# Kernel optimization log

Hardware: AMD Instinct MI355X
Metric: run time of the kernel (lower is better)

Reference implementation:

```python
import jax, jax.numpy as jnp
import numpy as np

WORD_LEN = 4094
MAX_LEN = 9
EMB = 512
HID = 256
BATCH = 32768


def setup_inputs() -> dict:
    key = jax.random.key(0)
    ks = jax.random.split(key, 16)
    s = 0.02
    return {
        "decode_word": jax.random.randint(ks[0], (BATCH, 1), 0, WORD_LEN),
        "hidden": jax.random.normal(ks[1], (BATCH, HID), jnp.float32),
        "encoder_output": jax.random.normal(ks[2], (BATCH, MAX_LEN, HID), jnp.float32),
        "emb_table": jax.random.normal(ks[3], (WORD_LEN, EMB), jnp.float32) * s,
        "atten_W": jax.random.normal(ks[4], (MAX_LEN, 2 * HID), jnp.float32) * s,
        "atten_b": jnp.zeros((MAX_LEN,), jnp.float32),
        "comb_W": jax.random.normal(ks[5], (EMB, EMB + HID), jnp.float32) * s,
        "comb_b": jnp.zeros((EMB,), jnp.float32),
        "W_ih": jax.random.normal(ks[6], (3 * HID, EMB), jnp.float32) * s,
        "b_ih": jnp.zeros((3 * HID,), jnp.float32),
        "W_hh": jax.random.normal(ks[7], (3 * HID, HID), jnp.float32) * s,
        "b_hh": jnp.zeros((3 * HID,), jnp.float32),
        "out_W": jax.random.normal(ks[8], (WORD_LEN, HID), jnp.float32) * s,
        "out_b": jnp.zeros((WORD_LEN,), jnp.float32),
    }


def reference(decode_word, hidden, encoder_output, emb_table, atten_W, atten_b,
              comb_W, comb_b, W_ih, b_ih, W_hh, b_hh, out_W, out_b):
    # embedding: [B,1,E]
    embedded = emb_table[decode_word]
    B = hidden.shape[0]
    # expand hidden to [B,L,H], concat with encoder_output -> attention scores [B,L,L]
    hx = jnp.broadcast_to(hidden[:, None, :], (B, MAX_LEN, HID))
    scores = jnp.einsum('blf,mf->blm', jnp.concatenate([encoder_output, hx], axis=2), atten_W) + atten_b
    atten_weight = jax.nn.softmax(scores, axis=2)
    # bmm: [B,L,L] @ [B,L,H] -> [B,L,H], then sum over L -> context [B,1,H]
    atten_applied = jnp.einsum('blm,bmh->blh', atten_weight, encoder_output)
    c_i = atten_applied.sum(axis=1)[:, None, :]
    # combine + relu: [B,1,E]
    x = jnp.concatenate([embedded, c_i], axis=2) @ comb_W.T + comb_b
    x = jax.nn.relu(x)[:, 0]  # [B,E]
    # GRUCell (PyTorch gate order: r, z, n)
    gi = x @ W_ih.T + b_ih
    gh = hidden @ W_hh.T + b_hh
    i_r, i_z, i_n = jnp.split(gi, 3, axis=1)
    h_r, h_z, h_n = jnp.split(gh, 3, axis=1)
    r = jax.nn.sigmoid(i_r + h_r)
    z = jax.nn.sigmoid(i_z + h_z)
    n = jnp.tanh(i_n + r * h_n)
    h_new = (1.0 - z) * n + z * hidden
    # output projection + log_softmax over vocab
    out = jax.nn.log_softmax(h_new @ out_W.T + out_b, axis=1)
    return out, h_new
```

## Files before the change

### kernel.cpp

```cpp
#include <hip/hip_runtime.h>

typedef __bf16 bf16x8 __attribute__((ext_vector_type(8)));
typedef float  f32x4  __attribute__((ext_vector_type(4)));

#define BATCH_ 32768
#define VOC 4094
#define LGT_STRIDE 8188

__device__ inline unsigned short f2bf(float f) {
    unsigned int u = __builtin_bit_cast(unsigned int, f);
    unsigned int r = u + 0x7FFFu + ((u >> 16) & 1u);
    return (unsigned short)(r >> 16);
}
__device__ inline float bf2f(unsigned short u) {
    unsigned int v = ((unsigned int)u) << 16;
    return __builtin_bit_cast(float, v);
}
__device__ inline f32x4 mfma16(bf16x8 a, bf16x8 b, f32x4 c) {
    return __builtin_amdgcn_mfma_f32_16x16x32_bf16(a, b, c, 0, 0, 0);
}
__device__ inline void gload16(const void* g, void* l) {
    __builtin_amdgcn_global_load_lds(
        (const __attribute__((address_space(1))) void*)(g),
        (__attribute__((address_space(3))) void*)(l),
        16, 0, 0);
}

__global__ __launch_bounds__(256) void k_prep(
    const float* __restrict__ comb_W, const float* __restrict__ W_ih,
    const float* __restrict__ W_hh, const float* __restrict__ out_W,
    const float* __restrict__ b_ih, const float* __restrict__ b_hh,
    const float* __restrict__ out_b,
    unsigned short* __restrict__ cwb, unsigned short* __restrict__ wg2,
    unsigned short* __restrict__ owb, float* __restrict__ bg,
    float* __restrict__ obp) {
    int i = blockIdx.x * 256 + threadIdx.x;
    if (i < 512 * 768) {
        int n = i / 768, k = i - n * 768;
        int by = n >> 7, r = n & 127, kc = k >> 7, kl = k & 127;
        int dst = (by * 6 + kc) * 16384 + r * 128 + (((kl >> 3) ^ (r & 7)) << 3) + (kl & 7);
        cwb[dst] = f2bf(comb_W[i]);
    }
    if (i < 1024 * 768) {
        int row = i / 768, k = i - row * 768;
        int hgrp = row >> 6, g = (row >> 4) & 3, hl = row & 15;
        int h = hgrp * 16 + hl;
        float v;
        if (g == 0) v = (k < 512) ? W_ih[(size_t)h * 512 + k] : W_hh[(size_t)h * 256 + (k - 512)];
        else if (g == 1) v = (k < 512) ? W_ih[(size_t)(256 + h) * 512 + k] : W_hh[(size_t)(256 + h) * 256 + (k - 512)];
        else if (g == 2) v = (k < 512) ? W_ih[(size_t)(512 + h) * 512 + k] : 0.f;
        else v = (k < 512) ? 0.f : W_hh[(size_t)(512 + h) * 256 + (k - 512)];
        int by = row >> 7, r = row & 127, kc = k >> 7, kl = k & 127;
        int dst = (by * 6 + kc) * 16384 + r * 128 + (((kl >> 3) ^ (r & 7)) << 3) + (kl & 7);
        wg2[dst] = f2bf(v);
    }
    if (i < 4096 * 256) {
        int n = i >> 8, k = i & 255;
        int by = n >> 7, r = n & 127, kc = k >> 7, kl = k & 127;
        int dst = (by * 2 + kc) * 16384 + r * 128 + (((kl >> 3) ^ (r & 7)) << 3) + (kl & 7);
        owb[dst] = (n < VOC) ? f2bf(out_W[i]) : (unsigned short)0;
    }
    if (i < 1024) {
        float v = (i < 512) ? (b_ih[i] + b_hh[i]) : ((i < 768) ? b_ih[i] : b_hh[i - 256]);
        bg[i] = v;
    }
    if (i < 4096) obp[i] = (i < VOC) ? out_b[i] : -1.0e30f;
}

__global__ __launch_bounds__(256) void k_attn(
    const int* __restrict__ dw, const float* __restrict__ hidden,
    const float* __restrict__ enc, const float* __restrict__ emb,
    const float* __restrict__ aW, const float* __restrict__ ab,
    unsigned short* __restrict__ xcat, unsigned short* __restrict__ xh) {
    __shared__ float sAW[9 * 516];
    __shared__ float sAB[9];
    int tid = threadIdx.x;
    for (int i = tid; i < 9 * 512; i += 256) {
        int m = i >> 9, k = i & 511;
        sAW[m * 516 + k] = aW[i];
    }
    if (tid < 9) sAB[tid] = ab[tid];
    __syncthreads();
    int w = tid >> 6, lane = tid & 63;
    int b = blockIdx.x * 4 + w;
    const float* encb = enc + (size_t)b * (9 * 256);
    float4 h4 = *(const float4*)(hidden + (size_t)b * 256 + 4 * lane);

    float4 e[9];
#pragma unroll
    for (int l = 0; l < 9; l++) e[l] = *(const float4*)(encb + l * 256 + 4 * lane);

    float u[9];
#pragma unroll
    for (int m = 0; m < 9; m++) {
        float4 a = *(const float4*)&sAW[m * 516 + 256 + 4 * lane];
        float v = h4.x * a.x + h4.y * a.y + h4.z * a.z + h4.w * a.w;
        v += __shfl_xor(v, 1);  v += __shfl_xor(v, 2);  v += __shfl_xor(v, 4);
        v += __shfl_xor(v, 8);  v += __shfl_xor(v, 16); v += __shfl_xor(v, 32);
        u[m] = v + sAB[m];
    }
    float wsum[9] = {0, 0, 0, 0, 0, 0, 0, 0, 0};
#pragma unroll
    for (int l = 0; l < 9; l++) {
        float p[9];
#pragma unroll
        for (int m = 0; m < 9; m++) {
            float4 a = *(const float4*)&sAW[m * 516 + 4 * lane];
            float v = e[l].x * a.x + e[l].y * a.y + e[l].z * a.z + e[l].w * a.w;
            v += __shfl_xor(v, 1);  v += __shfl_xor(v, 2);  v += __shfl_xor(v, 4);
            v += __shfl_xor(v, 8);  v += __shfl_xor(v, 16); v += __shfl_xor(v, 32);
            p[m] = v + u[m];
        }
        float mx = p[0];
#pragma unroll
        for (int m = 1; m < 9; m++) mx = fmaxf(mx, p[m]);
        float s = 0.f, ex[9];
#pragma unroll
        for (int m = 0; m < 9; m++) { ex[m] = __expf(p[m] - mx); s += ex[m]; }
        float inv = 1.f / s;
#pragma unroll
        for (int m = 0; m < 9; m++) wsum[m] += ex[m] * inv;
    }
    float c0 = 0, c1 = 0, c2 = 0, c3 = 0;
#pragma unroll
    for (int m = 0; m < 9; m++) {
        c0 += wsum[m] * e[m].x; c1 += wsum[m] * e[m].y;
        c2 += wsum[m] * e[m].z; c3 += wsum[m] * e[m].w;
    }
    ushort4 cb; cb.x = f2bf(c0); cb.y = f2bf(c1); cb.z = f2bf(c2); cb.w = f2bf(c3);
    *(ushort4*)(xcat + (size_t)b * 768 + 512 + 4 * lane) = cb;
    ushort4 hb; hb.x = f2bf(h4.x); hb.y = f2bf(h4.y); hb.z = f2bf(h4.z); hb.w = f2bf(h4.w);
    *(ushort4*)(xh + (size_t)b * 768 + 512 + 4 * lane) = hb;

    int word = dw[b];
    const float* er = emb + (size_t)word * 512 + 8 * lane;
    float4 e0 = *(const float4*)er;
    float4 e1 = *(const float4*)(er + 4);
    ushort4 w0; w0.x = f2bf(e0.x); w0.y = f2bf(e0.y); w0.z = f2bf(e0.z); w0.w = f2bf(e0.w);
    ushort4 w1; w1.x = f2bf(e1.x); w1.y = f2bf(e1.y); w1.z = f2bf(e1.z); w1.w = f2bf(e1.w);
    *(ushort4*)(xcat + (size_t)b * 768 + 8 * lane) = w0;
    *(ushort4*)(xcat + (size_t)b * 768 + 8 * lane + 4) = w1;
}

__global__ __launch_bounds__(256, 2) void k_combine(
    const unsigned short* __restrict__ xcat, const unsigned short* __restrict__ cwb,
    const float* __restrict__ comb_b, unsigned short* __restrict__ xh) {
    __shared__ __align__(16) char smem[65536];
    int wgid = blockIdx.x;
    int xcd = wgid & 7, slot = wgid >> 3;
    int bx = xcd * 32 + (slot & 31), by = slot >> 5;
    int tid = threadIdx.x, w = tid >> 6, lane = tid & 63;
    int lo = lane & 15, hi = lane >> 4;
    int bm0 = bx * 128, n0 = by * 128;
    const __bf16* A = (const __bf16*)xcat;
    const char* gb = (const char*)cwb + (size_t)by * 6 * 32768;
    f32x4 acc[2][8] = {};
    bf16x8 Afb[2][2][4];
#pragma unroll
    for (int mf = 0; mf < 2; mf++)
#pragma unroll
        for (int ks = 0; ks < 4; ks++)
            Afb[0][mf][ks] = *(const bf16x8*)(A + (size_t)(bm0 + w * 32 + mf * 16 + lo) * 768 + ks * 32 + 8 * hi);
    for (int it = 0; it < 8; it++) {
        int uo = ((w * 8 + it) << 10);
        gload16(gb + uo + lane * 16, smem + uo);
    }
    __syncthreads();
#pragma unroll
    for (int c = 0; c < 6; c++) {
        if (c < 5) {
#pragma unroll
            for (int mf = 0; mf < 2; mf++)
#pragma unroll
                for (int ks = 0; ks < 4; ks++)
                    Afb[(c + 1) & 1][mf][ks] = *(const bf16x8*)(A + (size_t)(bm0 + w * 32 + mf * 16 + lo) * 768 + (c + 1) * 128 + ks * 32 + 8 * hi);
            const char* gc = gb + (size_t)(c + 1) * 32768;
            int boff = ((c + 1) & 1) * 32768;
            for (int it = 0; it < 8; it++) {
                int uo = ((w * 8 + it) << 10);
                gload16(gc + uo + lane * 16, smem + boff + uo);
            }
            __builtin_amdgcn_sched_barrier(0);
        }
        int cb0 = (c & 1) * 32768;
#pragma unroll
        for (int ks = 0; ks < 4; ks++)
#pragma unroll
            for (int nf = 0; nf < 8; nf++) {
                int row = nf * 16 + lo;
                bf16x8 bfr = *(const bf16x8*)(smem + cb0 + row * 256 + (((ks * 4 + hi) ^ (lo & 7)) << 4));
                acc[0][nf] = mfma16(Afb[c & 1][0][ks], bfr, acc[0][nf]);
                acc[1][nf] = mfma16(Afb[c & 1][1][ks], bfr, acc[1][nf]);
            }
        __syncthreads();
    }
#pragma unroll
    for (int mf = 0; mf < 2; mf++)
#pragma unroll
        for (int nf = 0; nf < 8; nf++) {
            int col = n0 + nf * 16 + lo;
            float cb = comb_b[col];
#pragma unroll
            for (int r = 0; r < 4; r++) {
                int row = bm0 + w * 32 + mf * 16 + hi * 4 + r;
                xh[(size_t)row * 768 + col] = f2bf(fmaxf(acc[mf][nf][r] + cb, 0.f));
            }
        }
}

__global__ __launch_bounds__(256, 2) void k_gru(
    const unsigned short* __restrict__ xh, const unsigned short* __restrict__ wg2,
    const float* __restrict__ bg, const float* __restrict__ hidden,
    float* __restrict__ hnew_out, unsigned short* __restrict__ hnb) {
    __shared__ __align__(16) char smem[65536];
    int wgid = blockIdx.x;
    int xcd = wgid & 7, slot = wgid >> 3;
    int bx = xcd * 32 + (slot & 31), by = slot >> 5;
    int tid = threadIdx.x, w = tid >> 6, lane = tid & 63;
    int lo = lane & 15, hi = lane >> 4;
    int bm0 = bx * 128;
    int h00 = by * 32;
    const __bf16* A = (const __bf16*)xh;
    const char* gb = (const char*)wg2 + (size_t)by * 6 * 32768;
    f32x4 acc[2][8] = {};
    bf16x8 Afb[2][2][4];
#pragma unroll
    for (int mf = 0; mf < 2; mf++)
#pragma unroll
        for (int ks = 0; ks < 4; ks++)
            Afb[0][mf][ks] = *(const bf16x8*)(A + (size_t)(bm0 + w * 32 + mf * 16 + lo) * 768 + ks * 32 + 8 * hi);
    for (int it = 0; it < 8; it++) {
        int uo = ((w * 8 + it) << 10);
        gload16(gb + uo + lane * 16, smem + uo);
    }
    __syncthreads();
#pragma unroll
    for (int c = 0; c < 6; c++) {
        if (c < 5) {
#pragma unroll
            for (int mf = 0; mf < 2; mf++)
#pragma unroll
                for (int ks = 0; ks < 4; ks++)
                    Afb[(c + 1) & 1][mf][ks] = *(const bf16x8*)(A + (size_t)(bm0 + w * 32 + mf * 16 + lo) * 768 + (c + 1) * 128 + ks * 32 + 8 * hi);
            const char* gc = gb + (size_t)(c + 1) * 32768;
            int boff = ((c + 1) & 1) * 32768;
            for (int it = 0; it < 8; it++) {
                int uo = ((w * 8 + it) << 10);
                gload16(gc + uo + lane * 16, smem + boff + uo);
            }
            __builtin_amdgcn_sched_barrier(0);
        }
        int cb0 = (c & 1) * 32768;
#pragma unroll
        for (int ks = 0; ks < 4; ks++)
#pragma unroll
            for (int nf = 0; nf < 8; nf++) {
                int row = nf * 16 + lo;
                bf16x8 bfr = *(const bf16x8*)(smem + cb0 + row * 256 + (((ks * 4 + hi) ^ (lo & 7)) << 4));
                acc[0][nf] = mfma16(Afb[c & 1][0][ks], bfr, acc[0][nf]);
                acc[1][nf] = mfma16(Afb[c & 1][1][ks], bfr, acc[1][nf]);
            }
        __syncthreads();
    }
#pragma unroll
    for (int mf = 0; mf < 2; mf++)
#pragma unroll
        for (int hgrp = 0; hgrp < 2; hgrp++) {
            int col = h00 + hgrp * 16 + lo;
            float br = bg[col], bz = bg[256 + col], bi = bg[512 + col], bh = bg[768 + col];
#pragma unroll
            for (int r = 0; r < 4; r++) {
                int row = bm0 + w * 32 + mf * 16 + hi * 4 + r;
                float rr = 1.f / (1.f + __expf(-(acc[mf][hgrp * 4 + 0][r] + br)));
                float zz = 1.f / (1.f + __expf(-(acc[mf][hgrp * 4 + 1][r] + bz)));
                float nn = tanhf(acc[mf][hgrp * 4 + 2][r] + bi + rr * (acc[mf][hgrp * 4 + 3][r] + bh));
                float hp = hidden[(size_t)row * 256 + col];
                float hn = zz * (hp - nn) + nn;
                hnew_out[(size_t)row * 256 + col] = hn;
                hnb[(size_t)row * 256 + col] = f2bf(hn);
            }
        }
}

__global__ __launch_bounds__(256, 2) void k_logit(
    const unsigned short* __restrict__ hnb, const unsigned short* __restrict__ owb,
    const float* __restrict__ obp, unsigned short* __restrict__ lgt,
    float* __restrict__ psum) {
    __shared__ __align__(16) char smem[65536];
    int wgid = blockIdx.x;
    int xcd = wgid & 7, slot = wgid >> 3;
    int bx = xcd * 32 + (slot & 31), by = slot >> 5;
    int tid = threadIdx.x, w = tid >> 6, lane = tid & 63;
    int lo = lane & 15, hi = lane >> 4;
    int bm0 = bx * 128, n0 = by * 128;
    const __bf16* A = (const __bf16*)hnb;
    const char* gb = (const char*)owb + (size_t)by * 2 * 32768;

    for (int it = 0; it < 8; it++) {
        int uo = ((w * 8 + it) << 10);
        gload16(gb + uo + lane * 16, smem + uo);
    }
    bf16x8 Af[2][8];
#pragma unroll
    for (int mf = 0; mf < 2; mf++)
#pragma unroll
        for (int ks = 0; ks < 8; ks++)
            Af[mf][ks] = *(const bf16x8*)(A + (size_t)(bm0 + w * 32 + mf * 16 + lo) * 256 + ks * 32 + 8 * hi);
    __syncthreads();
    for (int it = 0; it < 8; it++) {
        int uo = ((w * 8 + it) << 10);
        gload16(gb + 32768 + uo + lane * 16, smem + 32768 + uo);
    }
    __builtin_amdgcn_sched_barrier(0);

    f32x4 acc[2][8] = {};
#pragma unroll
    for (int ks = 0; ks < 4; ks++)
#pragma unroll
        for (int nf = 0; nf < 8; nf++) {
            int row = nf * 16 + lo;
            bf16x8 bfr = *(const bf16x8*)(smem + row * 256 + (((ks * 4 + hi) ^ (lo & 7)) << 4));
            acc[0][nf] = mfma16(Af[0][ks], bfr, acc[0][nf]);
            acc[1][nf] = mfma16(Af[1][ks], bfr, acc[1][nf]);
        }
    __syncthreads();
#pragma unroll
    for (int ks = 4; ks < 8; ks++)
#pragma unroll
        for (int nf = 0; nf < 8; nf++) {
            int row = nf * 16 + lo;
            bf16x8 bfr = *(const bf16x8*)(smem + 32768 + row * 256 + ((((ks - 4) * 4 + hi) ^ (lo & 7)) << 4));
            acc[0][nf] = mfma16(Af[0][ks], bfr, acc[0][nf]);
            acc[1][nf] = mfma16(Af[1][ks], bfr, acc[1][nf]);
        }
    __syncthreads();

    unsigned short* T = (unsigned short*)smem;
    float se[2][4] = {};
#pragma unroll
    for (int mf = 0; mf < 2; mf++)
#pragma unroll
        for (int nf = 0; nf < 8; nf++) {
            int col = n0 + nf * 16 + lo;
            float ob = obp[col];
#pragma unroll
            for (int r = 0; r < 4; r++) {
                float lg = acc[mf][nf][r] + ob;
                se[mf][r] += __expf(lg);
                T[(w * 32 + mf * 16 + hi * 4 + r) * 136 + nf * 16 + lo] = f2bf(lg);
            }
        }
#pragma unroll
    for (int mf = 0; mf < 2; mf++)
#pragma unroll
        for (int r = 0; r < 4; r++) {
            float v = se[mf][r];
            v += __shfl_xor(v, 1); v += __shfl_xor(v, 2);
            v += __shfl_xor(v, 4); v += __shfl_xor(v, 8);
            se[mf][r] = v;
        }
    if (lo == 0) {
#pragma unroll
        for (int mf = 0; mf < 2; mf++)
#pragma unroll
            for (int r = 0; r < 4; r++)
                psum[(size_t)by * BATCH_ + bm0 + w * 32 + mf * 16 + hi * 4 + r] = se[mf][r];
    }
    __syncthreads();
#pragma unroll
    for (int it = 0; it < 8; it++) {
        int t = it * 256 + tid;
        int row = t >> 4, ch = t & 15;
        ushort4 a = *(ushort4*)(T + row * 136 + ch * 8);
        ushort4 b = *(ushort4*)(T + row * 136 + ch * 8 + 4);
        size_t base = (size_t)(bm0 + row) * LGT_STRIDE + n0 + ch * 8;
        *(ushort4*)(lgt + base) = a;
        *(ushort4*)(lgt + base + 4) = b;
    }
}

__global__ __launch_bounds__(256) void k_lse(
    const float* __restrict__ psum, float* __restrict__ lse) {
    int b = blockIdx.x * 256 + threadIdx.x;
    float t = 0.f;
#pragma unroll
    for (int s = 0; s < 32; s++) t += psum[(size_t)s * BATCH_ + b];
    lse[b] = __logf(t);
}

__global__ __launch_bounds__(256) void k_out2(
    const float* __restrict__ lse, float* __restrict__ out) {
    int b = blockIdx.x, tid = threadIdx.x;
    float l = lse[b];
    const unsigned short* rowp = (const unsigned short*)(out + (size_t)b * VOC);
    ushort4 a0 = *(const ushort4*)(rowp + tid * 8);
    ushort4 b0 = *(const ushort4*)(rowp + tid * 8 + 4);
    ushort4 a1 = *(const ushort4*)(rowp + 2048 + tid * 8);
    ushort4 b1 = *(const ushort4*)(rowp + 2048 + tid * 8 + 4);
    __syncthreads();
    float* orow = out + (size_t)b * VOC;
    int v0 = tid * 8;
    {
        float2 p;
        p.x = bf2f(a0.x) - l; p.y = bf2f(a0.y) - l; *(float2*)(orow + v0) = p;
        p.x = bf2f(a0.z) - l; p.y = bf2f(a0.w) - l; *(float2*)(orow + v0 + 2) = p;
        p.x = bf2f(b0.x) - l; p.y = bf2f(b0.y) - l; *(float2*)(orow + v0 + 4) = p;
        p.x = bf2f(b0.z) - l; p.y = bf2f(b0.w) - l; *(float2*)(orow + v0 + 6) = p;
    }
    int v1 = 2048 + tid * 8;
    {
        float2 p;
        p.x = bf2f(a1.x) - l; p.y = bf2f(a1.y) - l;
        if (v1 + 1 < VOC) *(float2*)(orow + v1) = p;
        p.x = bf2f(a1.z) - l; p.y = bf2f(a1.w) - l;
        if (v1 + 3 < VOC) *(float2*)(orow + v1 + 2) = p;
        p.x = bf2f(b1.x) - l; p.y = bf2f(b1.y) - l;
        if (v1 + 5 < VOC) *(float2*)(orow + v1 + 4) = p;
        p.x = bf2f(b1.z) - l; p.y = bf2f(b1.w) - l;
        if (v1 + 7 < VOC) *(float2*)(orow + v1 + 6) = p;
    }
}

extern "C" void kernel_launch(void* const* d_in, const int* in_sizes, int n_in,
                              void* d_out, int out_size, void* d_ws, size_t ws_size,
                              hipStream_t stream) {
    const int*   dw      = (const int*)d_in[0];
    const float* hidden  = (const float*)d_in[1];
    const float* enc     = (const float*)d_in[2];
    const float* emb     = (const float*)d_in[3];
    const float* aW      = (const float*)d_in[4];
    const float* ab      = (const float*)d_in[5];
    const float* comb_W  = (const float*)d_in[6];
    const float* comb_b  = (const float*)d_in[7];
    const float* W_ih    = (const float*)d_in[8];
    const float* b_ih    = (const float*)d_in[9];
    const float* W_hh    = (const float*)d_in[10];
    const float* b_hh    = (const float*)d_in[11];
    const float* out_W   = (const float*)d_in[12];
    const float* out_b   = (const float*)d_in[13];

    float* out = (float*)d_out;
    float* hnew_out = out + (size_t)BATCH_ * VOC;

    unsigned short* xcat = (unsigned short*)d_ws;
    unsigned short* xh   = xcat + (size_t)BATCH_ * 768;
    unsigned short* hnb  = xh + (size_t)BATCH_ * 768;
    float* psum          = (float*)(hnb + (size_t)BATCH_ * 256);
    float* lse           = psum + (size_t)32 * BATCH_;
    float* obp           = lse + BATCH_;
    unsigned short* cwb  = (unsigned short*)(obp + 4096);
    unsigned short* wg2  = cwb + 512 * 768;
    unsigned short* owb  = wg2 + 1024 * 768;
    float* bg            = (float*)(owb + 4096 * 256);

    k_prep<<<4096, 256, 0, stream>>>(comb_W, W_ih, W_hh, out_W, b_ih, b_hh, out_b,
                                     cwb, wg2, owb, bg, obp);
    k_attn<<<BATCH_ / 4, 256, 0, stream>>>(dw, hidden, enc, emb, aW, ab, xcat, xh);
    k_combine<<<1024, 256, 0, stream>>>(xcat, cwb, comb_b, xh);
    k_gru<<<2048, 256, 0, stream>>>(xh, wg2, bg, hidden, hnew_out, hnb);
    k_logit<<<8192, 256, 0, stream>>>(hnb, owb, obp, (unsigned short*)out, psum);
    k_lse<<<BATCH_ / 256, 256, 0, stream>>>(psum, lse);
    k_out2<<<BATCH_, 256, 0, stream>>>(lse, out);
}
```

Before: 839.1 us.

## Halve GEMM K-chunk to 64 for 4 blocks/CU and fuse lse into output

Repacks all bf16 weight tiles with a 64-wide K chunk, which halves the LDS footprint of the combine, GRU and logit GEMMs. Launch bounds rise from 2 to 4 blocks per CU, so more waves can hide memory latency. The logit kernel becomes a double-buffered four-stage pipeline with prefetched A fragments instead of holding the whole A row in registers. The separate log-sum-exp kernel is folded into the final output kernel using a warp-shuffle reduction, saving one launch. In exchange there are twice as many barrier-separated K iterations, and the higher occupancy target may cause register spills.

```diff
diff --git a/kernel.cpp b/kernel.cpp
--- a/kernel.cpp
+++ b/kernel.cpp
@@ -37,8 +37,8 @@
     int i = blockIdx.x * 256 + threadIdx.x;
     if (i < 512 * 768) {
         int n = i / 768, k = i - n * 768;
-        int by = n >> 7, r = n & 127, kc = k >> 7, kl = k & 127;
-        int dst = (by * 6 + kc) * 16384 + r * 128 + (((kl >> 3) ^ (r & 7)) << 3) + (kl & 7);
+        int by = n >> 7, r = n & 127, kc = k >> 6, kl = k & 63;
+        int dst = (by * 12 + kc) * 8192 + r * 64 + (((kl >> 3) ^ (r & 7)) << 3) + (kl & 7);
         cwb[dst] = f2bf(comb_W[i]);
     }
     if (i < 1024 * 768) {
@@ -50,14 +50,14 @@
         else if (g == 1) v = (k < 512) ? W_ih[(size_t)(256 + h) * 512 + k] : W_hh[(size_t)(256 + h) * 256 + (k - 512)];
         else if (g == 2) v = (k < 512) ? W_ih[(size_t)(512 + h) * 512 + k] : 0.f;
         else v = (k < 512) ? 0.f : W_hh[(size_t)(512 + h) * 256 + (k - 512)];
-        int by = row >> 7, r = row & 127, kc = k >> 7, kl = k & 127;
-        int dst = (by * 6 + kc) * 16384 + r * 128 + (((kl >> 3) ^ (r & 7)) << 3) + (kl & 7);
+        int by = row >> 7, r = row & 127, kc = k >> 6, kl = k & 63;
+        int dst = (by * 12 + kc) * 8192 + r * 64 + (((kl >> 3) ^ (r & 7)) << 3) + (kl & 7);
         wg2[dst] = f2bf(v);
     }
     if (i < 4096 * 256) {
         int n = i >> 8, k = i & 255;
-        int by = n >> 7, r = n & 127, kc = k >> 7, kl = k & 127;
-        int dst = (by * 2 + kc) * 16384 + r * 128 + (((kl >> 3) ^ (r & 7)) << 3) + (kl & 7);
+        int by = n >> 7, r = n & 127, kc = k >> 6, kl = k & 63;
+        int dst = (by * 4 + kc) * 8192 + r * 64 + (((kl >> 3) ^ (r & 7)) << 3) + (kl & 7);
         owb[dst] = (n < VOC) ? f2bf(out_W[i]) : (unsigned short)0;
     }
     if (i < 1024) {
@@ -142,10 +142,10 @@
     *(ushort4*)(xcat + (size_t)b * 768 + 8 * lane + 4) = w1;
 }
 
-__global__ __launch_bounds__(256, 2) void k_combine(
+__global__ __launch_bounds__(256, 4) void k_combine(
     const unsigned short* __restrict__ xcat, const unsigned short* __restrict__ cwb,
     const float* __restrict__ comb_b, unsigned short* __restrict__ xh) {
-    __shared__ __align__(16) char smem[65536];
+    __shared__ __align__(16) char smem[32768];
     int wgid = blockIdx.x;
     int xcd = wgid & 7, slot = wgid >> 3;
     int bx = xcd * 32 + (slot & 31), by = slot >> 5;
@@ -153,44 +153,45 @@
     int lo = lane & 15, hi = lane >> 4;
     int bm0 = bx * 128, n0 = by * 128;
     const __bf16* A = (const __bf16*)xcat;
-    const char* gb = (const char*)cwb + (size_t)by * 6 * 32768;
+    const char* gb = (const char*)cwb + (size_t)by * 12 * 16384;
+    size_t ar = (size_t)(bm0 + w * 32 + lo) * 768 + 8 * hi;
     f32x4 acc[2][8] = {};
-    bf16x8 Afb[2][2][4];
-#pragma unroll
-    for (int mf = 0; mf < 2; mf++)
-#pragma unroll
-        for (int ks = 0; ks < 4; ks++)
-            Afb[0][mf][ks] = *(const bf16x8*)(A + (size_t)(bm0 + w * 32 + mf * 16 + lo) * 768 + ks * 32 + 8 * hi);
-    for (int it = 0; it < 8; it++) {
-        int uo = ((w * 8 + it) << 10);
+    bf16x8 Afb[2][2][2];
+#pragma unroll
+    for (int mf = 0; mf < 2; mf++)
+#pragma unroll
+        for (int ks = 0; ks < 2; ks++)
+            Afb[0][mf][ks] = *(const bf16x8*)(A + ar + mf * 16 * 768 + ks * 32);
+    for (int it = 0; it < 4; it++) {
+        int uo = (w * 4 + it) << 10;
         gload16(gb + uo + lane * 16, smem + uo);
     }
     __syncthreads();
 #pragma unroll
-    for (int c = 0; c < 6; c++) {
-        if (c < 5) {
+    for (int c = 0; c < 12; c++) {
+        int cur = c & 1;
+        if (c < 11) {
+            const char* gc = gb + (size_t)(c + 1) * 16384;
+            char* lb = smem + (cur ^ 1) * 16384;
+            for (int it = 0; it < 4; it++) {
+                int uo = (w * 4 + it) << 10;
+                gload16(gc + uo + lane * 16, lb + uo);
+            }
 #pragma unroll
             for (int mf = 0; mf < 2; mf++)
 #pragma unroll
-                for (int ks = 0; ks < 4; ks++)
-                    Afb[(c + 1) & 1][mf][ks] = *(const bf16x8*)(A + (size_t)(bm0 + w * 32 + mf * 16 + lo) * 768 + (c + 1) * 128 + ks * 32 + 8 * hi);
-            const char* gc = gb + (size_t)(c + 1) * 32768;
-            int boff = ((c + 1) & 1) * 32768;
-            for (int it = 0; it < 8; it++) {
-                int uo = ((w * 8 + it) << 10);
-                gload16(gc + uo + lane * 16, smem + boff + uo);
-            }
-            __builtin_amdgcn_sched_barrier(0);
-        }
-        int cb0 = (c & 1) * 32768;
-#pragma unroll
-        for (int ks = 0; ks < 4; ks++)
+                for (int ks = 0; ks < 2; ks++)
+                    Afb[cur ^ 1][mf][ks] = *(const bf16x8*)(A + ar + mf * 16 * 768 + (c + 1) * 64 + ks * 32);
+        }
+        const char* cb = smem + cur * 16384;
+#pragma unroll
+        for (int ks = 0; ks < 2; ks++)
 #pragma unroll
             for (int nf = 0; nf < 8; nf++) {
                 int row = nf * 16 + lo;
-                bf16x8 bfr = *(const bf16x8*)(smem + cb0 + row * 256 + (((ks * 4 + hi) ^ (lo & 7)) << 4));
-                acc[0][nf] = mfma16(Afb[c & 1][0][ks], bfr, acc[0][nf]);
-                acc[1][nf] = mfma16(Afb[c & 1][1][ks], bfr, acc[1][nf]);
+                bf16x8 bfr = *(const bf16x8*)(cb + row * 128 + (((ks * 4 + hi) ^ (lo & 7)) << 4));
+                acc[0][nf] = mfma16(Afb[cur][0][ks], bfr, acc[0][nf]);
+                acc[1][nf] = mfma16(Afb[cur][1][ks], bfr, acc[1][nf]);
             }
         __syncthreads();
     }
@@ -208,11 +209,11 @@
         }
 }
 
-__global__ __launch_bounds__(256, 2) void k_gru(
+__global__ __launch_bounds__(256, 4) void k_gru(
     const unsigned short* __restrict__ xh, const unsigned short* __restrict__ wg2,
     const float* __restrict__ bg, const float* __restrict__ hidden,
     float* __restrict__ hnew_out, unsigned short* __restrict__ hnb) {
-    __shared__ __align__(16) char smem[65536];
+    __shared__ __align__(16) char smem[32768];
     int wgid = blockIdx.x;
     int xcd = wgid & 7, slot = wgid >> 3;
     int bx = xcd * 32 + (slot & 31), by = slot >> 5;
@@ -221,44 +222,45 @@
     int bm0 = bx * 128;
     int h00 = by * 32;
     const __bf16* A = (const __bf16*)xh;
-    const char* gb = (const char*)wg2 + (size_t)by * 6 * 32768;
+    const char* gb = (const char*)wg2 + (size_t)by * 12 * 16384;
+    size_t ar = (size_t)(bm0 + w * 32 + lo) * 768 + 8 * hi;
     f32x4 acc[2][8] = {};
-    bf16x8 Afb[2][2][4];
-#pragma unroll
-    for (int mf = 0; mf < 2; mf++)
-#pragma unroll
-        for (int ks = 0; ks < 4; ks++)
-            Afb[0][mf][ks] = *(const bf16x8*)(A + (size_t)(bm0 + w * 32 + mf * 16 + lo) * 768 + ks * 32 + 8 * hi);
-    for (int it = 0; it < 8; it++) {
-        int uo = ((w * 8 + it) << 10);
+    bf16x8 Afb[2][2][2];
+#pragma unroll
+    for (int mf = 0; mf < 2; mf++)
+#pragma unroll
+        for (int ks = 0; ks < 2; ks++)
+            Afb[0][mf][ks] = *(const bf16x8*)(A + ar + mf * 16 * 768 + ks * 32);
+    for (int it = 0; it < 4; it++) {
+        int uo = (w * 4 + it) << 10;
         gload16(gb + uo + lane * 16, smem + uo);
     }
     __syncthreads();
 #pragma unroll
-    for (int c = 0; c < 6; c++) {
-        if (c < 5) {
+    for (int c = 0; c < 12; c++) {
+        int cur = c & 1;
+        if (c < 11) {
+            const char* gc = gb + (size_t)(c + 1) * 16384;
+            char* lb = smem + (cur ^ 1) * 16384;
+            for (int it = 0; it < 4; it++) {
+                int uo = (w * 4 + it) << 10;
+                gload16(gc + uo + lane * 16, lb + uo);
+            }
 #pragma unroll
             for (int mf = 0; mf < 2; mf++)
 #pragma unroll
-                for (int ks = 0; ks < 4; ks++)
-                    Afb[(c + 1) & 1][mf][ks] = *(const bf16x8*)(A + (size_t)(bm0 + w * 32 + mf * 16 + lo) * 768 + (c + 1) * 128 + ks * 32 + 8 * hi);
-            const char* gc = gb + (size_t)(c + 1) * 32768;
-            int boff = ((c + 1) & 1) * 32768;
-            for (int it = 0; it < 8; it++) {
-                int uo = ((w * 8 + it) << 10);
-                gload16(gc + uo + lane * 16, smem + boff + uo);
-            }
-            __builtin_amdgcn_sched_barrier(0);
-        }
-        int cb0 = (c & 1) * 32768;
-#pragma unroll
-        for (int ks = 0; ks < 4; ks++)
+                for (int ks = 0; ks < 2; ks++)
+                    Afb[cur ^ 1][mf][ks] = *(const bf16x8*)(A + ar + mf * 16 * 768 + (c + 1) * 64 + ks * 32);
+        }
+        const char* cb = smem + cur * 16384;
+#pragma unroll
+        for (int ks = 0; ks < 2; ks++)
 #pragma unroll
             for (int nf = 0; nf < 8; nf++) {
                 int row = nf * 16 + lo;
-                bf16x8 bfr = *(const bf16x8*)(smem + cb0 + row * 256 + (((ks * 4 + hi) ^ (lo & 7)) << 4));
-                acc[0][nf] = mfma16(Afb[c & 1][0][ks], bfr, acc[0][nf]);
-                acc[1][nf] = mfma16(Afb[c & 1][1][ks], bfr, acc[1][nf]);
+                bf16x8 bfr = *(const bf16x8*)(cb + row * 128 + (((ks * 4 + hi) ^ (lo & 7)) << 4));
+                acc[0][nf] = mfma16(Afb[cur][0][ks], bfr, acc[0][nf]);
+                acc[1][nf] = mfma16(Afb[cur][1][ks], bfr, acc[1][nf]);
             }
         __syncthreads();
     }
@@ -282,11 +284,11 @@
         }
 }
 
-__global__ __launch_bounds__(256, 2) void k_logit(
+__global__ __launch_bounds__(256, 4) void k_logit(
     const unsigned short* __restrict__ hnb, const unsigned short* __restrict__ owb,
     const float* __restrict__ obp, unsigned short* __restrict__ lgt,
     float* __restrict__ psum) {
-    __shared__ __align__(16) char smem[65536];
+    __shared__ __align__(16) char smem[34816];
     int wgid = blockIdx.x;
     int xcd = wgid & 7, slot = wgid >> 3;
     int bx = xcd * 32 + (slot & 31), by = slot >> 5;
@@ -294,46 +296,48 @@
     int lo = lane & 15, hi = lane >> 4;
     int bm0 = bx * 128, n0 = by * 128;
     const __bf16* A = (const __bf16*)hnb;
-    const char* gb = (const char*)owb + (size_t)by * 2 * 32768;
-
-    for (int it = 0; it < 8; it++) {
-        int uo = ((w * 8 + it) << 10);
+    const char* gb = (const char*)owb + (size_t)by * 4 * 16384;
+    size_t ar = (size_t)(bm0 + w * 32 + lo) * 256 + 8 * hi;
+    f32x4 acc[2][8] = {};
+    bf16x8 Afb[2][2][2];
+#pragma unroll
+    for (int mf = 0; mf < 2; mf++)
+#pragma unroll
+        for (int ks = 0; ks < 2; ks++)
+            Afb[0][mf][ks] = *(const bf16x8*)(A + ar + mf * 16 * 256 + ks * 32);
+    for (int it = 0; it < 4; it++) {
+        int uo = (w * 4 + it) << 10;
         gload16(gb + uo + lane * 16, smem + uo);
     }
-    bf16x8 Af[2][8];
-#pragma unroll
-    for (int mf = 0; mf < 2; mf++)
-#pragma unroll
-        for (int ks = 0; ks < 8; ks++)
-            Af[mf][ks] = *(const bf16x8*)(A + (size_t)(bm0 + w * 32 + mf * 16 + lo) * 256 + ks * 32 + 8 * hi);
-    __syncthreads();
-    for (int it = 0; it < 8; it++) {
-        int uo = ((w * 8 + it) << 10);
-        gload16(gb + 32768 + uo + lane * 16, smem + 32768 + uo);
-    }
-    __builtin_amdgcn_sched_barrier(0);
-
-    f32x4 acc[2][8] = {};
-#pragma unroll
-    for (int ks = 0; ks < 4; ks++)
-#pragma unroll
-        for (int nf = 0; nf < 8; nf++) {
-            int row = nf * 16 + lo;
-            bf16x8 bfr = *(const bf16x8*)(smem + row * 256 + (((ks * 4 + hi) ^ (lo & 7)) << 4));
-            acc[0][nf] = mfma16(Af[0][ks], bfr, acc[0][nf]);
-            acc[1][nf] = mfma16(Af[1][ks], bfr, acc[1][nf]);
-        }
-    __syncthreads();
-#pragma unroll
-    for (int ks = 4; ks < 8; ks++)
-#pragma unroll
-        for (int nf = 0; nf < 8; nf++) {
-            int row = nf * 16 + lo;
-            bf16x8 bfr = *(const bf16x8*)(smem + 32768 + row * 256 + ((((ks - 4) * 4 + hi) ^ (lo & 7)) << 4));
-            acc[0][nf] = mfma16(Af[0][ks], bfr, acc[0][nf]);
-            acc[1][nf] = mfma16(Af[1][ks], bfr, acc[1][nf]);
-        }
-    __syncthreads();
+    __syncthreads();
+#pragma unroll
+    for (int c = 0; c < 4; c++) {
+        int cur = c & 1;
+        if (c < 3) {
+            const char* gc = gb + (size_t)(c + 1) * 16384;
+            char* lb = smem + (cur ^ 1) * 16384;
+            for (int it = 0; it < 4; it++) {
+                int uo = (w * 4 + it) << 10;
+                gload16(gc + uo + lane * 16, lb + uo);
+            }
+#pragma unroll
+            for (int mf = 0; mf < 2; mf++)
+#pragma unroll
+                for (int ks = 0; ks < 2; ks++)
+                    Afb[cur ^ 1][mf][ks] = *(const bf16x8*)(A + ar + mf * 16 * 256 + (c + 1) * 64 + ks * 32);
+        }
+        const char* cb = smem + cur * 16384;
+#pragma unroll
+        for (int ks = 0; ks < 2; ks++)
+#pragma unroll
+            for (int nf = 0; nf < 8; nf++) {
+                int row = nf * 16 + lo;
+                bf16x8 bfr = *(const bf16x8*)(cb + row * 128 + (((ks * 4 + hi) ^ (lo & 7)) << 4));
+                acc[0][nf] = mfma16(Afb[cur][0][ks], bfr, acc[0][nf]);
+                acc[1][nf] = mfma16(Afb[cur][1][ks], bfr, acc[1][nf]);
+            }
+        __syncthreads();
+    }
 
     unsigned short* T = (unsigned short*)smem;
     float se[2][4] = {};
@@ -379,25 +383,23 @@
     }
 }
 
-__global__ __launch_bounds__(256) void k_lse(
-    const float* __restrict__ psum, float* __restrict__ lse) {
-    int b = blockIdx.x * 256 + threadIdx.x;
-    float t = 0.f;
-#pragma unroll
-    for (int s = 0; s < 32; s++) t += psum[(size_t)s * BATCH_ + b];
-    lse[b] = __logf(t);
-}
-
 __global__ __launch_bounds__(256) void k_out2(
-    const float* __restrict__ lse, float* __restrict__ out) {
+    const float* __restrict__ psum, float* __restrict__ out) {
+    __shared__ float sl;
     int b = blockIdx.x, tid = threadIdx.x;
-    float l = lse[b];
     const unsigned short* rowp = (const unsigned short*)(out + (size_t)b * VOC);
     ushort4 a0 = *(const ushort4*)(rowp + tid * 8);
     ushort4 b0 = *(const ushort4*)(rowp + tid * 8 + 4);
     ushort4 a1 = *(const ushort4*)(rowp + 2048 + tid * 8);
     ushort4 b1 = *(const ushort4*)(rowp + 2048 + tid * 8 + 4);
-    __syncthreads();
+    if (tid < 32) {
+        float v = psum[(size_t)tid * BATCH_ + b];
+        v += __shfl_xor(v, 1); v += __shfl_xor(v, 2); v += __shfl_xor(v, 4);
+        v += __shfl_xor(v, 8); v += __shfl_xor(v, 16);
+        if (tid == 0) sl = __logf(v);
+    }
+    __syncthreads();
+    float l = sl;
     float* orow = out + (size_t)b * VOC;
     int v0 = tid * 8;
     {
@@ -446,8 +448,7 @@
     unsigned short* xh   = xcat + (size_t)BATCH_ * 768;
     unsigned short* hnb  = xh + (size_t)BATCH_ * 768;
     float* psum          = (float*)(hnb + (size_t)BATCH_ * 256);
-    float* lse           = psum + (size_t)32 * BATCH_;
-    float* obp           = lse + BATCH_;
+    float* obp           = psum + (size_t)32 * BATCH_;
     unsigned short* cwb  = (unsigned short*)(obp + 4096);
     unsigned short* wg2  = cwb + 512 * 768;
     unsigned short* owb  = wg2 + 1024 * 768;
@@ -459,6 +460,5 @@
     k_combine<<<1024, 256, 0, stream>>>(xcat, cwb, comb_b, xh);
     k_gru<<<2048, 256, 0, stream>>>(xh, wg2, bg, hidden, hnew_out, hnb);
     k_logit<<<8192, 256, 0, stream>>>(hnb, owb, obp, (unsigned short*)out, psum);
-    k_lse<<<BATCH_ / 256, 256, 0, stream>>>(psum, lse);
-    k_out2<<<BATCH_, 256, 0, stream>>>(lse, out);
-}
+    k_out2<<<BATCH_, 256, 0, stream>>>(psum, out);
+}
```

Result: faster. 760.2 us (-9.4%).
